# Kernel optimization log

Measured on AMD Instinct MI355X. Metric: run time of the kernel, lower is better.

The kernel has to match this reference:

```python
import jax, jax.numpy as jnp
import numpy as np

TOUT = 4096  # fixed padded output frame length (>= max possible cumsum of durations)


def setup_inputs() -> dict:
    key = jax.random.key(0)
    k1, k2 = jax.random.split(key)
    xs = jax.random.normal(k1, (8, 512, 384), dtype=jnp.float32)
    ds = jax.random.randint(k2, (8, 512), 0, 8, dtype=jnp.int64)
    return {"xs": xs, "ds": ds}


def reference(xs, ds):
    # xs: (B, Tin, D) phoneme embeddings; ds: (B, Tin) integer durations.
    # Build mapping matrix M: (B, Tout, Tin) where M[b, t, i] = 1 iff frame t
    # falls in [cumsum(ds)[i] - ds[i], cumsum(ds)[i]), then ys = M @ xs.
    cum = jnp.cumsum(ds, axis=1)          # (B, Tin) right boundaries
    left = cum - ds                        # (B, Tin) left boundaries
    frames = jnp.arange(TOUT)              # (Tout,)
    f = frames[None, :, None]              # (1, Tout, 1)
    M = ((f >= left[:, None, :]) & (f < cum[:, None, :])).astype(xs.dtype)  # (B, Tout, Tin)
    ys = jnp.einsum('bti,bid->btd', M, xs)  # (B, Tout, D)
    return ys
```

## Files before the change

kernel.cpp:

```cpp
#include <hip/hip_runtime.h>

#define NB   8
#define NIN  512
#define TOUT 4096
#define ND   384

__global__ __launch_bounds__(NIN) void build_idx(const int* __restrict__ ds,
                                                 int* __restrict__ idx) {
    const int b   = blockIdx.x;
    const int tid = threadIdx.x;
    __shared__ int s[NIN];

    const int d = ds[b * NIN + tid];
    s[tid] = d;

    #pragma unroll
    for (int t = tid; t < TOUT; t += NIN) idx[b * TOUT + t] = -1;
    __syncthreads();

    #pragma unroll
    for (int off = 1; off < NIN; off <<= 1) {
        int v = (tid >= off) ? s[tid - off] : 0;
        __syncthreads();
        s[tid] += v;
        __syncthreads();
    }

    int right = s[tid];
    int left  = right - d;
    if (right > TOUT) right = TOUT;
    for (int t = left; t < right; ++t) idx[b * TOUT + t] = tid;
}

__global__ __launch_bounds__(256) void gather(const float4* __restrict__ xs,
                                              const int* __restrict__ idx,
                                              float4* __restrict__ out) {
    const int J = ND / 4;
    unsigned gid = blockIdx.x * blockDim.x + threadIdx.x;
    unsigned j   = gid % J;
    unsigned row = gid / J;
    int i = idx[row];
    float4 v = make_float4(0.f, 0.f, 0.f, 0.f);
    if (i >= 0) {
        unsigned b = row / TOUT;
        v = xs[(b * NIN + (unsigned)i) * J + j];
    }
    out[(unsigned long)row * J + j] = v;
}

extern "C" void kernel_launch(void* const* d_in, const int* in_sizes, int n_in,
                              void* d_out, int out_size, void* d_ws, size_t ws_size,
                              hipStream_t stream) {
    const float* xs = (const float*)d_in[0];
    const int*   ds = (const int*)d_in[1];
    float* out = (float*)d_out;
    int* idx = (int*)d_ws;

    build_idx<<<NB, NIN, 0, stream>>>(ds, idx);

    const unsigned total4 = NB * TOUT * (ND / 4);
    gather<<<total4 / 256, 256, 0, stream>>>((const float4*)xs, idx,
                                             (float4*)out);
}
```

Measured before the change: 76.77 us.

## Fuse index build into gather with per-block scan and binary search

Replaces the two-kernel scheme (serial build of a frame-to-phoneme index in workspace, then gather) with a single kernel. Each block redundantly computes the batch's duration prefix sum with wavefront shuffles, binary-searches the owner phoneme for its 32 output rows, then streams the rows. This removes a launch, the idx workspace round trip, and the slow single-block-per-batch index fill, at the cost of repeating the scan in every block.

```diff
diff --git a/kernel.cpp b/kernel.cpp
--- a/kernel.cpp
+++ b/kernel.cpp
@@ -1,51 +1,77 @@
 #include <hip/hip_runtime.h>
 
-#define NB   8
-#define NIN  512
-#define TOUT 4096
-#define ND   384
+#define NB    8
+#define NIN   512
+#define TOUT  4096
+#define ND    384
+#define J4    (ND / 4)
+#define TROWS 32
+#define BLK   256
 
-__global__ __launch_bounds__(NIN) void build_idx(const int* __restrict__ ds,
-                                                 int* __restrict__ idx) {
-    const int b   = blockIdx.x;
-    const int tid = threadIdx.x;
-    __shared__ int s[NIN];
+__global__ __launch_bounds__(BLK) void lenreg(const float4* __restrict__ xs,
+                                              const int* __restrict__ ds,
+                                              float4* __restrict__ out) {
+    const int b       = blockIdx.y;
+    const int rowbase = blockIdx.x * TROWS;
+    const int tid     = threadIdx.x;
 
-    const int d = ds[b * NIN + tid];
-    s[tid] = d;
+    __shared__ int cum[NIN];
+    __shared__ int wsum[BLK / 64];
+    __shared__ int owner[TROWS];
 
+    const int* dsb = ds + b * NIN;
+    const int a0 = dsb[2 * tid];
+    const int a1 = dsb[2 * tid + 1];
+    int p = a0 + a1;
+    const int lane = tid & 63;
+    const int wid  = tid >> 6;
     #pragma unroll
-    for (int t = tid; t < TOUT; t += NIN) idx[b * TOUT + t] = -1;
+    for (int off = 1; off < 64; off <<= 1) {
+        int v = __shfl_up(p, off, 64);
+        if (lane >= off) p += v;
+    }
+    if (lane == 63) wsum[wid] = p;
+    __syncthreads();
+    int acc = 0;
+    #pragma unroll
+    for (int w = 0; w < BLK / 64; ++w)
+        if (w < wid) acc += wsum[w];
+    p += acc;
+    cum[2 * tid + 1] = p;
+    cum[2 * tid]     = p - a1;
     __syncthreads();
 
+    const int total = cum[NIN - 1];
+    if (tid < TROWS) {
+        const int t = rowbase + tid;
+        int o = -1;
+        if (t < total) {
+            int lo = 0, hi = NIN;
+            #pragma unroll
+            for (int s = 0; s < 10; ++s) {
+                if (lo < hi) {
+                    int mid = (lo + hi) >> 1;
+                    if (cum[mid] > t) hi = mid; else lo = mid + 1;
+                }
+            }
+            o = lo;
+        }
+        owner[tid] = o;
+    }
+    __syncthreads();
+
+    const float4* xsb  = xs + (size_t)b * NIN * J4;
+    float4*       outb = out + ((size_t)b * TOUT + rowbase) * J4;
     #pragma unroll
-    for (int off = 1; off < NIN; off <<= 1) {
-        int v = (tid >= off) ? s[tid - off] : 0;
-        __syncthreads();
-        s[tid] += v;
-        __syncthreads();
+    for (int k = 0; k < TROWS * J4 / BLK; ++k) {
+        const int g = k * BLK + tid;
+        const int r = g / J4;
+        const int j = g - r * J4;
+        const int o = owner[r];
+        float4 v = make_float4(0.f, 0.f, 0.f, 0.f);
+        if (o >= 0) v = xsb[o * J4 + j];
+        outb[g] = v;
     }
-
-    int right = s[tid];
-    int left  = right - d;
-    if (right > TOUT) right = TOUT;
-    for (int t = left; t < right; ++t) idx[b * TOUT + t] = tid;
-}
-
-__global__ __launch_bounds__(256) void gather(const float4* __restrict__ xs,
-                                              const int* __restrict__ idx,
-                                              float4* __restrict__ out) {
-    const int J = ND / 4;
-    unsigned gid = blockIdx.x * blockDim.x + threadIdx.x;
-    unsigned j   = gid % J;
-    unsigned row = gid / J;
-    int i = idx[row];
-    float4 v = make_float4(0.f, 0.f, 0.f, 0.f);
-    if (i >= 0) {
-        unsigned b = row / TOUT;
-        v = xs[(b * NIN + (unsigned)i) * J + j];
-    }
-    out[(unsigned long)row * J + j] = v;
 }
 
 extern "C" void kernel_launch(void* const* d_in, const int* in_sizes, int n_in,
@@ -54,11 +80,7 @@
     const float* xs = (const float*)d_in[0];
     const int*   ds = (const int*)d_in[1];
     float* out = (float*)d_out;
-    int* idx = (int*)d_ws;
 
-    build_idx<<<NB, NIN, 0, stream>>>(ds, idx);
-
-    const unsigned total4 = NB * TOUT * (ND / 4);
-    gather<<<total4 / 256, 256, 0, stream>>>((const float4*)xs, idx,
-                                             (float4*)out);
+    dim3 grid(TOUT / TROWS, NB);
+    lenreg<<<grid, BLK, 0, stream>>>((const float4*)xs, ds, (float4*)out);
 }
```

Result: no change. 75.48 us (-1.7%).
